# Kernel optimization log

Hardware: AMD Instinct MI355X
Metric: run time of the kernel (lower is better)

## Reference

```python
import jax, jax.numpy as jnp
import numpy as np

V, E, H, T, B = 100000, 256, 256, 50, 512
FORGET_BIAS = 2.0


def setup_inputs() -> dict:
    key = jax.random.key(0)
    ks = jax.random.split(key, 12)
    s = 0.05
    return {
        "input_queries": jax.random.randint(ks[0], (B, T), 0, V, dtype=jnp.int32),
        "input_replies": jax.random.randint(ks[1], (B, T), 0, V, dtype=jnp.int32),
        "query_lengths": jax.random.randint(ks[2], (B,), 1, T, dtype=jnp.int32),
        "reply_lengths": jax.random.randint(ks[3], (B,), 1, T, dtype=jnp.int32),
        # keep weak distances strictly positive (diagonal is inverted)
        "weak_distances": jax.random.uniform(ks[4], (B, B), jnp.float32) + 0.5,
        "embeddings": jax.random.normal(ks[5], (V, E), jnp.float32) * s,
        "W": jax.random.normal(ks[6], (E + H, 4 * H), jnp.float32) * s,
        "b": jnp.zeros((4 * H,), jnp.float32),
        "p_i": jax.random.normal(ks[7], (H,), jnp.float32) * s,
        "p_f": jax.random.normal(ks[8], (H,), jnp.float32) * s,
        "p_o": jax.random.normal(ks[9], (H,), jnp.float32) * s,
        "M": jax.random.normal(ks[10], (H, H), jnp.float32) * s,
    }


def lstm_encode(x, lengths, W, b, p_i, p_f, p_o):
    """TF LSTMCell(use_peepholes=True, forget_bias=2.0); returns final h at each
    sequence's length (dynamic_rnn semantics: state frozen past length)."""
    Bx, Tx, _ = x.shape
    Hx = p_i.shape[0]
    h0 = jnp.zeros((Bx, Hx), x.dtype)

    def step(carry, xt_t):
        xt, t = xt_t
        h, c = carry
        z = jnp.concatenate([xt, h], axis=-1) @ W + b  # [B, 4H]
        i, j, f, o = jnp.split(z, 4, axis=-1)
        i = jax.nn.sigmoid(i + p_i * c)
        f = jax.nn.sigmoid(f + FORGET_BIAS + p_f * c)
        c_new = f * c + i * jnp.tanh(j)
        o = jax.nn.sigmoid(o + p_o * c_new)
        h_new = o * jnp.tanh(c_new)
        m = (t < lengths)[:, None]
        return (jnp.where(m, h_new, h), jnp.where(m, c_new, c)), None

    (h, _), _ = jax.lax.scan(step, (h0, h0),
                             (jnp.swapaxes(x, 0, 1), jnp.arange(Tx)))
    return h


def reference(input_queries, input_replies, query_lengths, reply_lengths,
              weak_distances, embeddings, W, b, p_i, p_f, p_o, M):
    q_emb = embeddings[input_queries]  # [B, T, E]
    r_emb = embeddings[input_replies]  # [B, T, E]
    # query and reply cells share weights (reuse=True in the original)
    q = lstm_encode(q_emb, query_lengths, W, b, p_i, p_f, p_o)  # [B, H]
    r = lstm_encode(r_emb, reply_lengths, W, b, p_i, p_f, p_o)  # [B, H]
    q = q @ M
    distances = q @ r.T                      # [B, B]
    pos = jnp.diagonal(distances)            # positive logits, [B]
    wp = jnp.diagonal(weak_distances)        # [B]
    # wp_tiled[i, j] = wp[j]; positive_logits_tiled[i, j] = pos[j]
    wd_norm = jnp.maximum(0.0, weak_distances / wp[None, :] - 1.0)
    loss = jnp.sum(jnp.maximum(0.0, distances - pos[None, :] + wd_norm))
    return loss
```

## Files before the change

### kernel.cpp

```cpp
#include <hip/hip_runtime.h>

#define TTs 50
#define NSTEP 49

using short8   = __attribute__((ext_vector_type(8))) short;
using ushort4v = __attribute__((ext_vector_type(4))) unsigned short;
using f32x4    = __attribute__((ext_vector_type(4))) float;
using int4v    = __attribute__((ext_vector_type(4))) int;

__device__ __forceinline__ unsigned short f2bf(float f) {
    unsigned u = __builtin_bit_cast(unsigned, f);
    u += 0x7FFFu + ((u >> 16) & 1u);
    return (unsigned short)(u >> 16);
}
__device__ __forceinline__ float bf2f(unsigned short s) {
    unsigned u = ((unsigned)s) << 16;
    return __builtin_bit_cast(float, u);
}
__device__ __forceinline__ float frcp(float x) { return __builtin_amdgcn_rcpf(x); }
__device__ __forceinline__ float sigm(float x)  { return frcp(1.f + __expf(-x)); }
__device__ __forceinline__ float ftanh(float x) { return 1.f - 2.f * frcp(__expf(2.f * x) + 1.f); }

#define WH_SCALE 512.f
#define H_SCALE  127.f

__global__ __launch_bounds__(64)
void init_kernel(float* __restrict__ out) { if (threadIdx.x == 0) out[0] = 0.f; }

__global__ __launch_bounds__(256)
void pack_w_kernel(const float* __restrict__ W,
                   unsigned short* __restrict__ Wxp, signed char* __restrict__ Wq)
{
    __shared__ float ld[64][65];
    const int koff = blockIdx.y * 256;
    const int k0 = (blockIdx.x & 3) * 64, c0 = (blockIdx.x >> 2) * 64;
    const int tid = threadIdx.x;
    #pragma unroll
    for (int i = 0; i < 16; ++i) {
        int idx = tid + i * 256;
        ld[idx >> 6][idx & 63] = W[(size_t)(koff + k0 + (idx >> 6)) * 1024 + c0 + (idx & 63)];
    }
    __syncthreads();
    if (blockIdx.y == 0) {
        #pragma unroll
        for (int j = 0; j < 2; ++j) {
            int idx = tid + j * 256;
            int cl = idx >> 3, kc = (idx & 7) * 8;
            short8 v;
            #pragma unroll
            for (int e = 0; e < 8; ++e) v[e] = (short)f2bf(ld[kc + e][cl]);
            *(short8*)(Wxp + (size_t)(c0 + cl) * 256 + k0 + kc) = v;
        }
    } else {
        #pragma unroll
        for (int j = 0; j < 2; ++j) {
            int idx = tid + j * 256;
            int cl = idx >> 3, kc = (idx & 7) * 8;
            unsigned long long u = 0;
            #pragma unroll
            for (int e = 0; e < 8; ++e) {
                float v = ld[kc + e][cl] * WH_SCALE;
                int q = __float2int_rn(fminf(fmaxf(v, -127.f), 127.f));
                u |= (unsigned long long)(unsigned char)(signed char)q << (8 * e);
            }
            *(unsigned long long*)(Wq + (size_t)(c0 + cl) * 256 + k0 + kc) = u;
        }
    }
}

__global__ __launch_bounds__(512, 4)
void xproj_kernel(const float* __restrict__ emb,
                  const int* __restrict__ idq, const int* __restrict__ idr,
                  const int* __restrict__ lenq, const int* __restrict__ lenr,
                  const unsigned short* __restrict__ Wxp,
                  const float* __restrict__ bias,
                  unsigned short* __restrict__ X)
{
    __shared__ __align__(16) unsigned short As[64 * 264];
    __shared__ int Ls2[4][64];
    __shared__ int Ids2[4][64];

    const int tid = threadIdx.x;
    const int L = tid & 63, w = tid >> 6;
    const int lanelo = L & 15, lhi = L >> 4;
    const int cslice = blockIdx.y;
    const int colbase = cslice * 256 + w * 32;
    const int slot0 = cslice * 16 + w * 2;

    short8 Bx[2][8];
    #pragma unroll
    for (int cf = 0; cf < 2; ++cf) {
        const unsigned short* bb = Wxp + (size_t)(colbase + cf * 16 + lanelo) * 256 + lhi * 8;
        #pragma unroll
        for (int ks = 0; ks < 8; ++ks) Bx[cf][ks] = *(const short8*)(bb + ks * 32);
    }
    float bc[2];
    #pragma unroll
    for (int cf = 0; cf < 2; ++cf) {
        int col = colbase + cf * 16 + lanelo;
        bc[cf] = bias[col] + ((col >= 512 && col < 768) ? 2.0f : 0.f);
    }

    if (tid < 256) {
        int it = tid >> 6, rl = tid & 63;
        int rt = blockIdx.x + it * 196;
        int t = rt >> 4, r0 = (rt & 15) * 64;
        int gr = r0 + rl;
        Ls2[it][rl] = (gr < 512) ? lenq[gr] : lenr[gr - 512];
        Ids2[it][rl] = (gr < 512) ? idq[gr * TTs + t] : idr[(gr - 512) * TTs + t];
    }
    __syncthreads();

    for (int it = 0; it < 4; ++it) {
        const int rt = blockIdx.x + it * 196;
        const int t = rt >> 4;
        const int rblkb = (rt & 15) * 4;
        const int* Ls = Ls2[it];
        const int* Ids = Ids2[it];

        float4 ev0[4], ev1[4];
        bool live[4];
        #pragma unroll
        for (int i = 0; i < 4; ++i) {
            int task = tid + i * 512;
            int rl = task >> 5, kc = (task & 31) * 8;
            live[i] = (t < Ls[rl]);
            if (live[i]) {
                const float* ep = emb + (size_t)Ids[rl] * 256 + kc;
                ev0[i] = *(const float4*)ep;
                ev1[i] = *(const float4*)(ep + 4);
            }
        }
        #pragma unroll
        for (int i = 0; i < 4; ++i) {
            if (live[i]) {
                int task = tid + i * 512;
                int rl = task >> 5, kc = (task & 31) * 8;
                short8 v;
                v[0] = (short)f2bf(ev0[i].x); v[1] = (short)f2bf(ev0[i].y);
                v[2] = (short)f2bf(ev0[i].z); v[3] = (short)f2bf(ev0[i].w);
                v[4] = (short)f2bf(ev1[i].x); v[5] = (short)f2bf(ev1[i].y);
                v[6] = (short)f2bf(ev1[i].z); v[7] = (short)f2bf(ev1[i].w);
                *(short8*)(As + rl * 264 + kc) = v;
            }
        }
        __syncthreads();

        #pragma unroll
        for (int rg = 0; rg < 4; ++rg) {
            int base = rg * 16 + lhi * 4;
            int lmax = max(max(Ls[base], Ls[base + 1]), max(Ls[base + 2], Ls[base + 3]));
            bool myalive = (t < lmax);
            if (__any(myalive)) {
                f32x4 a0 = (f32x4){0.f, 0.f, 0.f, 0.f};
                f32x4 a1 = (f32x4){0.f, 0.f, 0.f, 0.f};
                const unsigned short* ar = As + (rg * 16 + lanelo) * 264 + lhi * 8;
                #pragma unroll
                for (int ks = 0; ks < 8; ++ks) {
                    short8 a = *(const short8*)(ar + ks * 32);
                    a0 = __builtin_amdgcn_mfma_f32_16x16x32_bf16(a, Bx[0][ks], a0, 0, 0, 0);
                    a1 = __builtin_amdgcn_mfma_f32_16x16x32_bf16(a, Bx[1][ks], a1, 0, 0, 0);
                }
                if (myalive) {
                    size_t off = (((size_t)(t * 64 + rblkb + rg)) * 64 + slot0) * 256 + L * 4;
                    ushort4v v0, v1;
                    #pragma unroll
                    for (int j = 0; j < 4; ++j) {
                        v0[j] = f2bf(a0[j] + bc[0]);
                        v1[j] = f2bf(a1[j] + bc[1]);
                    }
                    *(ushort4v*)(X + off) = v0;
                    *(ushort4v*)(X + off + 256) = v1;
                }
            }
        }
        __syncthreads();
    }
}

__global__ __launch_bounds__(1024, 4)
void lstm_i8_kernel(const unsigned short* __restrict__ X,
                    const signed char* __restrict__ Wq,
                    const float* __restrict__ p_i, const float* __restrict__ p_f,
                    const float* __restrict__ p_o,
                    const int* __restrict__ lenq, const int* __restrict__ lenr,
                    unsigned short* __restrict__ hfin)
{
    __shared__ int hl_i[2176];
    char* hlb = (char*)hl_i;
    const int tid = threadIdx.x;
    const int L = tid & 63, w = tid >> 6;
    const int blk = blockIdx.x;
    const int lanelo = L & 15, lhi = L >> 4;
    const int hh = w * 16 + lanelo;

    for (int i = tid; i < 2176; i += 1024) hl_i[i] = 0;

    int4v Bw[4][4];
    #pragma unroll
    for (int g = 0; g < 4; ++g)
        #pragma unroll
        for (int kc = 0; kc < 4; ++kc)
            Bw[g][kc] = *(const int4v*)(Wq + (size_t)(g * 256 + hh) * 256 + kc * 64 + lhi * 16);

    const unsigned short* xb = X + (size_t)(blk >> 2) * 16384;
    int xgoff[4];
    #pragma unroll
    for (int g = 0; g < 4; ++g)
        xgoff[g] = (g * 16 + w) * 256 + (blk & 3) * 64 + lanelo * 4 + lhi;

    const int ard = lanelo * 272 + lhi * 16;
    const int awr = (lhi * 4) * 272 + hh;

    const float pii = p_i[hh], pff = p_f[hh], poo = p_o[hh];
    const float INV = 1.f / (H_SCALE * WH_SCALE);

    const int gr = blk * 4 + lhi;
    const int len_ = (gr < 512) ? lenq[gr] : lenr[gr - 512];

    float cst = 0.f;
    float hst = 0.f;

    unsigned short xr[4], xn[4];
    #pragma unroll
    for (int g = 0; g < 4; ++g) xr[g] = xb[xgoff[g]];

    __syncthreads();

    for (int t = 0; t < NSTEP; ++t) {
        const int rb = (t & 1) * 4352;
        const int wb = 4352 - rb;

        const int tn = (t + 1 < NSTEP) ? t + 1 : NSTEP - 1;
        const unsigned short* xt1 = xb + (size_t)tn * 1048576;
        #pragma unroll
        for (int g = 0; g < 4; ++g) xn[g] = xt1[xgoff[g]];

        int4v acc[4];
        #pragma unroll
        for (int g = 0; g < 4; ++g) acc[g] = (int4v){0, 0, 0, 0};

        #pragma unroll
        for (int kc = 0; kc < 4; ++kc) {
            int4v a = *(const int4v*)(hlb + rb + ard + kc * 64);
            #pragma unroll
            for (int g = 0; g < 4; ++g)
                acc[g] = __builtin_amdgcn_mfma_i32_16x16x64_i8(a, Bw[g][kc], acc[g], 0, 0, 0);
        }

        {
            float cv = cst;
            float zi = fmaf((float)acc[0][0], INV, bf2f(xr[0]));
            float zj = fmaf((float)acc[1][0], INV, bf2f(xr[1]));
            float zf = fmaf((float)acc[2][0], INV, bf2f(xr[2]));
            float zo = fmaf((float)acc[3][0], INV, bf2f(xr[3]));
            float iv = sigm(fmaf(pii, cv, zi));
            float fv = sigm(fmaf(pff, cv, zf));
            float jv = ftanh(zj);
            float cn = fv * cv + iv * jv;
            float ov = sigm(fmaf(poo, cn, zo));
            float hn = ov * ftanh(cn);
            bool upd = (t < len_);
            if (upd) { cst = cn; hst = hn; }
            hlb[wb + awr] = (signed char)__float2int_rn(hst * H_SCALE);
        }
        __syncthreads();
        #pragma unroll
        for (int g = 0; g < 4; ++g) xr[g] = xn[g];
    }

    hfin[(size_t)gr * 256 + hh] = f2bf(hst);
}

#define TS 64
#define KT 16
#define LDW (TS + 4)

__global__ __launch_bounds__(256)
void gemm_qM_kernel(const unsigned short* __restrict__ hA, const float* __restrict__ B,
                    float* __restrict__ C)
{
    __shared__ float As[KT][LDW];
    __shared__ float Bs[KT][LDW];
    const int tid = threadIdx.x;
    const int tx = tid & 15, ty = tid >> 4;
    const int m0 = blockIdx.x * TS, n0 = blockIdx.y * TS;
    float acc[4][4] = {};
    for (int kk = 0; kk < 256; kk += KT) {
        #pragma unroll
        for (int i = 0; i < 4; ++i) {
            int l = tid + i * 256;
            As[l & 15][l >> 4] = bf2f(hA[(m0 + (l >> 4)) * 256 + kk + (l & 15)]);
            Bs[l >> 6][l & 63] = B[(kk + (l >> 6)) * 256 + n0 + (l & 63)];
        }
        __syncthreads();
        #pragma unroll
        for (int k = 0; k < KT; ++k) {
            float4 a4 = *(const float4*)&As[k][ty * 4];
            float4 b4 = *(const float4*)&Bs[k][tx * 4];
            float av[4] = {a4.x, a4.y, a4.z, a4.w};
            float bv[4] = {b4.x, b4.y, b4.z, b4.w};
            #pragma unroll
            for (int i = 0; i < 4; ++i)
                #pragma unroll
                for (int j = 0; j < 4; ++j)
                    acc[i][j] = fmaf(av[i], bv[j], acc[i][j]);
        }
        __syncthreads();
    }
    #pragma unroll
    for (int i = 0; i < 4; ++i) {
        float4 v = {acc[i][0], acc[i][1], acc[i][2], acc[i][3]};
        *(float4*)&C[(m0 + ty * 4 + i) * 256 + n0 + tx * 4] = v;
    }
}

__global__ __launch_bounds__(256)
void gemm_D_kernel(const float* __restrict__ A, const unsigned short* __restrict__ hB,
                   float* __restrict__ C)
{
    __shared__ float As[KT][LDW];
    __shared__ float Bs[KT][LDW];
    const int tid = threadIdx.x;
    const int tx = tid & 15, ty = tid >> 4;
    const int m0 = blockIdx.x * TS, n0 = blockIdx.y * TS;
    float acc[4][4] = {};
    for (int kk = 0; kk < 256; kk += KT) {
        #pragma unroll
        for (int i = 0; i < 4; ++i) {
            int l = tid + i * 256;
            As[l & 15][l >> 4] = A[(m0 + (l >> 4)) * 256 + kk + (l & 15)];
            Bs[l & 15][l >> 4] = bf2f(hB[(n0 + (l >> 4)) * 256 + kk + (l & 15)]);
        }
        __syncthreads();
        #pragma unroll
        for (int k = 0; k < KT; ++k) {
            float4 a4 = *(const float4*)&As[k][ty * 4];
            float4 b4 = *(const float4*)&Bs[k][tx * 4];
            float av[4] = {a4.x, a4.y, a4.z, a4.w};
            float bv[4] = {b4.x, b4.y, b4.z, b4.w};
            #pragma unroll
            for (int i = 0; i < 4; ++i)
                #pragma unroll
                for (int j = 0; j < 4; ++j)
                    acc[i][j] = fmaf(av[i], bv[j], acc[i][j]);
        }
        __syncthreads();
    }
    #pragma unroll
    for (int i = 0; i < 4; ++i) {
        float4 v = {acc[i][0], acc[i][1], acc[i][2], acc[i][3]};
        *(float4*)&C[(m0 + ty * 4 + i) * 512 + n0 + tx * 4] = v;
    }
}

__global__ __launch_bounds__(256)
void loss_kernel(const float* __restrict__ D, const float* __restrict__ wd,
                 float* __restrict__ out)
{
    int idx = blockIdx.x * 256 + threadIdx.x;
    int j = idx & 511;
    float d   = D[idx];
    float pos = D[j * 512 + j];
    float ww  = wd[idx];
    float wp  = wd[j * 512 + j];
    float wn  = fmaxf(0.f, fmaf(ww, frcp(wp), -1.f));
    float v   = fmaxf(0.f, d - pos + wn);
    #pragma unroll
    for (int o = 32; o > 0; o >>= 1) v += __shfl_down(v, o);
    __shared__ float sm[4];
    if ((threadIdx.x & 63) == 0) sm[threadIdx.x >> 6] = v;
    __syncthreads();
    if (threadIdx.x == 0) atomicAdd(out, sm[0] + sm[1] + sm[2] + sm[3]);
}

extern "C" void kernel_launch(void* const* d_in, const int* in_sizes, int n_in,
                              void* d_out, int out_size, void* d_ws, size_t ws_size,
                              hipStream_t stream) {
    const int*   idq  = (const int*)d_in[0];
    const int*   idr  = (const int*)d_in[1];
    const int*   lenq = (const int*)d_in[2];
    const int*   lenr = (const int*)d_in[3];
    const float* wd   = (const float*)d_in[4];
    const float* emb  = (const float*)d_in[5];
    const float* W    = (const float*)d_in[6];
    const float* bias = (const float*)d_in[7];
    const float* p_i  = (const float*)d_in[8];
    const float* p_f  = (const float*)d_in[9];
    const float* p_o  = (const float*)d_in[10];
    const float* Mm   = (const float*)d_in[11];
    float* out = (float*)d_out;

    char* ws = (char*)d_ws;
    unsigned short* X    = (unsigned short*)ws;
    char* p = ws + (size_t)NSTEP * 1048576 * 2;
    unsigned short* hfin = (unsigned short*)p;  p += 1024 * 256 * 2;
    unsigned short* Wxp  = (unsigned short*)p;  p += 1024 * 256 * 2;
    signed char*    Wq   = (signed char*)p;     p += 1024 * 256;
    float* qM = (float*)p;  p += 512 * 256 * 4;
    float* D  = (float*)p;

    init_kernel<<<1, 64, 0, stream>>>(out);
    pack_w_kernel<<<dim3(64, 2), 256, 0, stream>>>(W, Wxp, Wq);
    xproj_kernel<<<dim3(196, 4), 512, 0, stream>>>(emb, idq, idr, lenq, lenr,
                                                   Wxp, bias, X);
    lstm_i8_kernel<<<256, 1024, 0, stream>>>(X, Wq, p_i, p_f, p_o,
                                             lenq, lenr, hfin);
    gemm_qM_kernel<<<dim3(8, 4), 256, 0, stream>>>(hfin, Mm, qM);
    gemm_D_kernel<<<dim3(8, 8), 256, 0, stream>>>(qM, hfin + 512 * 256, D);
    loss_kernel<<<1024, 256, 0, stream>>>(D, wd, out);
}
```

Baseline: 161.2 us.

## Sort sequences by length and stop LSTM recurrence at per-block max length

A new single-block kernel counting-sorts all 1024 query and reply sequences by length, longest first, into a permutation. The input projection and the LSTM kernel then process rows in that order, and hfin is still written back at each original row index. Each LSTM block now loops only up to the longest sequence among its 4 rows instead of a fixed 49 steps. The projection skips tiles whose timestep is past the longest length in the tile. The shared h buffer is compacted so that only every fourth lane loads the A operand, and the others keep zeros. This cuts the serial recurrence work for short sequences, at the cost of an extra tiny kernel and indirect index loads.

```diff
diff --git a/kernel.cpp b/kernel.cpp
--- a/kernel.cpp
+++ b/kernel.cpp
@@ -24,8 +24,26 @@
 #define WH_SCALE 512.f
 #define H_SCALE  127.f
 
-__global__ __launch_bounds__(64)
-void init_kernel(float* __restrict__ out) { if (threadIdx.x == 0) out[0] = 0.f; }
+__global__ __launch_bounds__(1024)
+void sort_kernel(const int* __restrict__ lenq, const int* __restrict__ lenr,
+                 int* __restrict__ perm, float* __restrict__ out)
+{
+    __shared__ int cnt[64];
+    const int tid = threadIdx.x;
+    if (tid == 0) out[0] = 0.f;
+    if (tid < 64) cnt[tid] = 0;
+    __syncthreads();
+    const int l = (tid < 512) ? lenq[tid] : lenr[tid - 512];
+    atomicAdd(&cnt[l], 1);
+    __syncthreads();
+    if (tid == 0) {
+        int acc = 0;
+        for (int v = 49; v >= 1; --v) { int c = cnt[v]; cnt[v] = acc; acc += c; }
+    }
+    __syncthreads();
+    const int rank = atomicAdd(&cnt[l], 1);
+    perm[rank] = tid;
+}
 
 __global__ __launch_bounds__(256)
 void pack_w_kernel(const float* __restrict__ W,
@@ -72,6 +90,7 @@
 void xproj_kernel(const float* __restrict__ emb,
                   const int* __restrict__ idq, const int* __restrict__ idr,
                   const int* __restrict__ lenq, const int* __restrict__ lenr,
+                  const int* __restrict__ perm,
                   const unsigned short* __restrict__ Wxp,
                   const float* __restrict__ bias,
                   unsigned short* __restrict__ X)
@@ -79,6 +98,7 @@
     __shared__ __align__(16) unsigned short As[64 * 264];
     __shared__ int Ls2[4][64];
     __shared__ int Ids2[4][64];
+    __shared__ int Tmax[4];
 
     const int tid = threadIdx.x;
     const int L = tid & 63, w = tid >> 6;
@@ -105,9 +125,11 @@
         int it = tid >> 6, rl = tid & 63;
         int rt = blockIdx.x + it * 196;
         int t = rt >> 4, r0 = (rt & 15) * 64;
-        int gr = r0 + rl;
-        Ls2[it][rl] = (gr < 512) ? lenq[gr] : lenr[gr - 512];
+        int gr = perm[r0 + rl];
+        int len = (gr < 512) ? lenq[gr] : lenr[gr - 512];
+        Ls2[it][rl] = len;
         Ids2[it][rl] = (gr < 512) ? idq[gr * TTs + t] : idr[(gr - 512) * TTs + t];
+        if (rl == 0) Tmax[it] = len;
     }
     __syncthreads();
 
@@ -115,6 +137,7 @@
         const int rt = blockIdx.x + it * 196;
         const int t = rt >> 4;
         const int rblkb = (rt & 15) * 4;
+        if (t >= Tmax[it]) continue;
         const int* Ls = Ls2[it];
         const int* Ids = Ids2[it];
 
@@ -184,17 +207,17 @@
                     const float* __restrict__ p_i, const float* __restrict__ p_f,
                     const float* __restrict__ p_o,
                     const int* __restrict__ lenq, const int* __restrict__ lenr,
+                    const int* __restrict__ perm,
                     unsigned short* __restrict__ hfin)
 {
-    __shared__ int hl_i[2176];
-    char* hlb = (char*)hl_i;
+    __shared__ __align__(16) char hl[2 * 4 * 288];
     const int tid = threadIdx.x;
     const int L = tid & 63, w = tid >> 6;
     const int blk = blockIdx.x;
     const int lanelo = L & 15, lhi = L >> 4;
     const int hh = w * 16 + lanelo;
 
-    for (int i = tid; i < 2176; i += 1024) hl_i[i] = 0;
+    if (tid < 576) ((int*)hl)[tid] = 0;
 
     int4v Bw[4][4];
     #pragma unroll
@@ -209,44 +232,55 @@
     for (int g = 0; g < 4; ++g)
         xgoff[g] = (g * 16 + w) * 256 + (blk & 3) * 64 + lanelo * 4 + lhi;
 
-    const int ard = lanelo * 272 + lhi * 16;
-    const int awr = (lhi * 4) * 272 + hh;
+    const bool rdlane = (lanelo & 3) == 0;
+    const int ard = (lanelo >> 2) * 288 + lhi * 16;
+    const int awr = lhi * 288 + hh;
 
     const float pii = p_i[hh], pff = p_f[hh], poo = p_o[hh];
     const float INV = 1.f / (H_SCALE * WH_SCALE);
 
-    const int gr = blk * 4 + lhi;
+    const int gr = perm[blk * 4 + lhi];
     const int len_ = (gr < 512) ? lenq[gr] : lenr[gr - 512];
+    const int p0 = perm[blk * 4];
+    const int blkmax = (p0 < 512) ? lenq[p0] : lenr[p0 - 512];
 
     float cst = 0.f;
     float hst = 0.f;
 
+    int4v a[4];
+    #pragma unroll
+    for (int kc = 0; kc < 4; ++kc) a[kc] = (int4v){0, 0, 0, 0};
+
     unsigned short xr[4], xn[4];
     #pragma unroll
     for (int g = 0; g < 4; ++g) xr[g] = xb[xgoff[g]];
-
-    __syncthreads();
-
-    for (int t = 0; t < NSTEP; ++t) {
-        const int rb = (t & 1) * 4352;
-        const int wb = 4352 - rb;
-
-        const int tn = (t + 1 < NSTEP) ? t + 1 : NSTEP - 1;
-        const unsigned short* xt1 = xb + (size_t)tn * 1048576;
-        #pragma unroll
-        for (int g = 0; g < 4; ++g) xn[g] = xt1[xgoff[g]];
+    const unsigned short* xp = xb + 1048576;
+
+    __syncthreads();
+
+    for (int t = 0; t < blkmax; ++t) {
+        const int rb = (t & 1) * 1152;
+        const int wb = 1152 - rb;
+
+        const unsigned short* xs = (t + 1 < blkmax) ? xp : xb;
+        #pragma unroll
+        for (int g = 0; g < 4; ++g) xn[g] = xs[xgoff[g]];
+        xp += 1048576;
+
+        if (rdlane) {
+            #pragma unroll
+            for (int kc = 0; kc < 4; ++kc)
+                a[kc] = *(const int4v*)(hl + rb + ard + kc * 64);
+        }
 
         int4v acc[4];
         #pragma unroll
         for (int g = 0; g < 4; ++g) acc[g] = (int4v){0, 0, 0, 0};
-
-        #pragma unroll
-        for (int kc = 0; kc < 4; ++kc) {
-            int4v a = *(const int4v*)(hlb + rb + ard + kc * 64);
+        #pragma unroll
+        for (int kc = 0; kc < 4; ++kc)
             #pragma unroll
             for (int g = 0; g < 4; ++g)
-                acc[g] = __builtin_amdgcn_mfma_i32_16x16x64_i8(a, Bw[g][kc], acc[g], 0, 0, 0);
-        }
+                acc[g] = __builtin_amdgcn_mfma_i32_16x16x64_i8(a[kc], Bw[g][kc], acc[g], 0, 0, 0);
 
         {
             float cv = cst;
@@ -262,7 +296,7 @@
             float hn = ov * ftanh(cn);
             bool upd = (t < len_);
             if (upd) { cst = cn; hst = hn; }
-            hlb[wb + awr] = (signed char)__float2int_rn(hst * H_SCALE);
+            hl[wb + awr] = (signed char)__float2int_rn(hst * H_SCALE);
         }
         __syncthreads();
         #pragma unroll
@@ -398,14 +432,15 @@
     unsigned short* Wxp  = (unsigned short*)p;  p += 1024 * 256 * 2;
     signed char*    Wq   = (signed char*)p;     p += 1024 * 256;
     float* qM = (float*)p;  p += 512 * 256 * 4;
-    float* D  = (float*)p;
-
-    init_kernel<<<1, 64, 0, stream>>>(out);
+    float* D  = (float*)p;  p += 512 * 512 * 4;
+    int* perm = (int*)p;
+
+    sort_kernel<<<1, 1024, 0, stream>>>(lenq, lenr, perm, out);
     pack_w_kernel<<<dim3(64, 2), 256, 0, stream>>>(W, Wxp, Wq);
     xproj_kernel<<<dim3(196, 4), 512, 0, stream>>>(emb, idq, idr, lenq, lenr,
-                                                   Wxp, bias, X);
+                                                   perm, Wxp, bias, X);
     lstm_i8_kernel<<<256, 1024, 0, stream>>>(X, Wq, p_i, p_f, p_o,
-                                             lenq, lenr, hfin);
+                                             lenq, lenr, perm, hfin);
     gemm_qM_kernel<<<dim3(8, 4), 256, 0, stream>>>(hfin, Mm, qM);
     gemm_D_kernel<<<dim3(8, 8), 256, 0, stream>>>(qM, hfin + 512 * 256, D);
     loss_kernel<<<1024, 256, 0, stream>>>(D, wd, out);
```

Result: faster. 150.1 us (median of 2 runs) (-6.9%).
